# Kernel tuning notes

Measured on AMD Instinct MI355X. Metric: run time of the kernel, lower is better.

Reference implementation:

```python
import jax, jax.numpy as jnp
import numpy as np

B, NLB, NPB, SDIM = 128, 32, 160, 256  # complexes, ligand atoms, pocket CAs, scalar dim


def _uniform(key, shape, fan_in):
    # kaiming_uniform_(a=sqrt(5)) -> U(-1/sqrt(fan_in), 1/sqrt(fan_in))
    bound = 1.0 / np.sqrt(fan_in)
    return jax.random.uniform(key, shape, jnp.float32, -bound, bound)


def setup_inputs() -> dict:
    key = jax.random.key(0)
    k1, k2, k3, k4, k5 = jax.random.split(key, 5)
    NL, NP = B * NLB, B * NPB
    # block-diagonal cross adjacency: every ligand atom paired with every pocket CA
    # of the same complex (same as (batch_ligand[:,None]==batch_pocket[None,:]).nonzero().T)
    l = np.repeat(np.arange(NL, dtype=np.int32), NPB)
    p = (np.arange(B, dtype=np.int32)[:, None, None] * NPB
         + np.zeros((1, NLB, 1), dtype=np.int32)
         + np.arange(NPB, dtype=np.int32)[None, None, :]).reshape(-1)
    return {
        "s_ligand": jax.random.normal(k1, (NL, SDIM), jnp.float32),
        "s_pocket": jax.random.normal(k2, (NP, SDIM), jnp.float32),
        "l": jnp.asarray(l),
        "p": jnp.asarray(p),
        "W1": _uniform(k3, (SDIM // 2, SDIM), SDIM),
        "b1": jnp.zeros((SDIM // 2,), jnp.float32),
        "W2": _uniform(k4, (SDIM // 4, SDIM // 2), SDIM // 2),
        "b2": jnp.zeros((SDIM // 4,), jnp.float32),
        "W3": _uniform(k5, (1, SDIM // 4), SDIM // 4),
        "b3": jnp.zeros((1,), jnp.float32),
    }


def reference(s_ligand, s_pocket, l, p, W1, b1, W2, b2, W3, b3):
    # gather cross-pair embeddings and sum: s[e] = s_ligand[l[e]] + s_pocket[p[e]]
    s = s_ligand[l] + s_pocket[p]                      # [E, sdim]
    h = jax.nn.silu(s @ W1.T + b1)                     # [E, sdim/2]
    h = jax.nn.silu(h @ W2.T + b2)                     # [E, sdim/4]
    out = jax.nn.relu(h @ W3.T + b3)                   # [E, 1]
    return out.squeeze(-1)                             # [E]
```

## Files before the change

kernel.cpp:

```cpp
#include <hip/hip_runtime.h>
#include <hip/hip_bf16.h>


#define B_CPLX   128
#define NLB      32
#define NPB      160
#define SDIM     256
#define H1DIM    128
#define NL_TOT   (B_CPLX * NLB)
#define NP_TOT   (B_CPLX * NPB)
#define NROWS    (NL_TOT + NP_TOT)
#define E_TOT    (B_CPLX * NLB * NPB)

#define W1_LDS_STRIDE 264
#define JT_CHUNK 16
#define ZP_STRIDE 132

typedef __bf16 bf16x8 __attribute__((ext_vector_type(8)));
typedef unsigned short ushortx8 __attribute__((ext_vector_type(8)));
typedef unsigned short ushortx4 __attribute__((ext_vector_type(4)));
typedef unsigned uintx4 __attribute__((ext_vector_type(4)));
typedef float f32x4 __attribute__((ext_vector_type(4)));

__device__ __forceinline__ unsigned short f2bf(float f) {
    unsigned u = __builtin_bit_cast(unsigned, f);
    u += 0x7FFFu + ((u >> 16) & 1u);
    return (unsigned short)(u >> 16);
}

__device__ __forceinline__ unsigned perm_hi16u(unsigned u0, unsigned u1) {
    return __builtin_amdgcn_perm(u1, u0, 0x07060302u);
}

__device__ __forceinline__ unsigned pack2_rhu(float x0, float x1) {
    unsigned u0 = __builtin_bit_cast(unsigned, x0) + 0x8000u;
    unsigned u1 = __builtin_bit_cast(unsigned, x1) + 0x8000u;
    return perm_hi16u(u0, u1);
}

__device__ __forceinline__ bf16x8 pack8_rhu(const float* x) {
    uintx4 h;
#pragma unroll
    for (int j = 0; j < 4; ++j) h[j] = pack2_rhu(x[2 * j], x[2 * j + 1]);
    return __builtin_bit_cast(bf16x8, h);
}

__device__ __forceinline__ void pack_split(const float* x, bf16x8& hi, bf16x8& lo) {
    uintx4 h, l;
#pragma unroll
    for (int j = 0; j < 4; ++j) {
        float x0 = x[2 * j], x1 = x[2 * j + 1];
        unsigned u0 = __builtin_bit_cast(unsigned, x0);
        unsigned u1 = __builtin_bit_cast(unsigned, x1);
        h[j] = perm_hi16u(u0, u1);
        float hf0 = __builtin_bit_cast(float, u0 & 0xFFFF0000u);
        float hf1 = __builtin_bit_cast(float, u1 & 0xFFFF0000u);
        l[j] = pack2_rhu(x0 - hf0, x1 - hf1);
    }
    hi = __builtin_bit_cast(bf16x8, h);
    lo = __builtin_bit_cast(bf16x8, l);
}

__device__ __forceinline__ float fast_silu(float x) {
    return x * __builtin_amdgcn_rcpf(1.0f + __expf(-x));
}

__device__ __forceinline__ float rowsum16(float s) {
    int b;
    b = __builtin_bit_cast(int, s);
    b = __builtin_amdgcn_update_dpp(b, b, 0x121, 0xF, 0xF, false);
    s += __builtin_bit_cast(float, b);
    b = __builtin_bit_cast(int, s);
    b = __builtin_amdgcn_update_dpp(b, b, 0x122, 0xF, 0xF, false);
    s += __builtin_bit_cast(float, b);
    b = __builtin_bit_cast(int, s);
    b = __builtin_amdgcn_update_dpp(b, b, 0x124, 0xF, 0xF, false);
    s += __builtin_bit_cast(float, b);
    b = __builtin_bit_cast(int, s);
    b = __builtin_amdgcn_update_dpp(b, b, 0x128, 0xF, 0xF, false);
    s += __builtin_bit_cast(float, b);
    return s;
}

__global__ __launch_bounds__(256) void proj_kernel(
    const float* __restrict__ s_lig, const float* __restrict__ s_poc,
    const float* __restrict__ W1,    const float* __restrict__ b1,
    float* __restrict__ Z)
{
    __shared__ unsigned short w1s[64 * W1_LDS_STRIDE];

    const int tid  = threadIdx.x;
    const int tg   = blockIdx.x >> 1;
    const int half = blockIdx.x & 1;

    {
        const f32x4* w4 = (const f32x4*)(W1 + (size_t)half * 64 * SDIM);
#pragma unroll
        for (int r = 0; r < 2; ++r) {
            f32x4 t[8];
#pragma unroll
            for (int s = 0; s < 8; ++s) t[s] = w4[tid + (r * 8 + s) * 256];
#pragma unroll
            for (int s = 0; s < 8; ++s) {
                const int u = tid + (r * 8 + s) * 256;
                const int n = u >> 6;
                const int k4 = u & 63;
                ushortx4 us;
#pragma unroll
                for (int j = 0; j < 4; ++j) us[j] = f2bf(t[s][j]);
                *(ushortx4*)(&w1s[n * W1_LDS_STRIDE + k4 * 4]) = us;
            }
        }
    }
    __syncthreads();

    const int lane = tid & 63;
    const int widx = tid >> 6;
    const int c    = lane & 15;
    const int q    = lane >> 4;
    const int tile = tg * 4 + widx;
    const int row  = tile * 16 + c;

    const float* src = (row < NL_TOT) ? (s_lig + (size_t)row * SDIM)
                                      : (s_poc + (size_t)(row - NL_TOT) * SDIM);

    f32x4 acc[4];
#pragma unroll
    for (int nt = 0; nt < 4; ++nt) acc[nt] = (f32x4){0.f, 0.f, 0.f, 0.f};

#pragma unroll
    for (int ks = 0; ks < 8; ++ks) {
        const int k0 = ks * 32 + q * 8;
        f32x4 xa = *reinterpret_cast<const f32x4*>(src + k0);
        f32x4 xb = *reinterpret_cast<const f32x4*>(src + k0 + 4);
        float xv[8] = {xa[0], xa[1], xa[2], xa[3], xb[0], xb[1], xb[2], xb[3]};
        bf16x8 ahi, alo;
        pack_split(xv, ahi, alo);
        bf16x8 bfrag[4];
#pragma unroll
        for (int nt = 0; nt < 4; ++nt)
            bfrag[nt] = *reinterpret_cast<const bf16x8*>(
                &w1s[(nt * 16 + c) * W1_LDS_STRIDE + k0]);
#pragma unroll
        for (int nt = 0; nt < 4; ++nt)
            acc[nt] = __builtin_amdgcn_mfma_f32_16x16x32_bf16(ahi, bfrag[nt], acc[nt], 0, 0, 0);
#pragma unroll
        for (int nt = 0; nt < 4; ++nt)
            acc[nt] = __builtin_amdgcn_mfma_f32_16x16x32_bf16(alo, bfrag[nt], acc[nt], 0, 0, 0);
    }

    const int mb = tile * 16 + q * 4;
#pragma unroll
    for (int nt = 0; nt < 4; ++nt) {
        const int n = half * 64 + nt * 16 + c;
        const float bias = b1[n];
#pragma unroll
        for (int r = 0; r < 4; ++r) {
            const int m = mb + r;
            float v = acc[nt][r];
            if (m < NL_TOT) v += bias;
            Z[(size_t)m * H1DIM + n] = v;
        }
    }
}

__global__ __launch_bounds__(256) void edge_kernel(
    const float* __restrict__ Z,
    const float* __restrict__ W2, const float* __restrict__ b2,
    const float* __restrict__ W3, const float* __restrict__ b3,
    float* __restrict__ out)
{
    __shared__ float zp[JT_CHUNK * ZP_STRIDE];
    __shared__ unsigned short w2s[16 * 64 * 8];

    const int tid = threadIdx.x;
    const int bid = blockIdx.x;
    const int b   = bid / 20;
    const int rem = bid - b * 20;
    const int jt  = rem >> 1;
    const int ih  = rem & 1;

    {
        const float* zpg = Z + (size_t)(NL_TOT + b * NPB + jt * JT_CHUNK) * H1DIM;
#pragma unroll
        for (int s = 0; s < 2; ++s) {
            const int u   = tid + s * 256;
            const int row = u >> 5;
            const int c4  = u & 31;
            f32x4 v = *(const f32x4*)(zpg + (size_t)row * H1DIM + c4 * 4);
            *(f32x4*)(&zp[row * ZP_STRIDE + c4 * 4]) = v;
        }
    }

    {
#pragma unroll
        for (int s = 0; s < 4; ++s) {
            const int slot   = tid + s * 256;
            const int lane_s = slot & 63;
            const int chunk  = slot >> 6;
            const int nt     = chunk >> 2;
            const int ks     = chunk & 3;
            const int n      = nt * 16 + (lane_s & 15);
            const int k0     = ks * 32 + (lane_s >> 4) * 8;
            const float* wsrc = W2 + (size_t)n * H1DIM + k0;
            f32x4 wa = *(const f32x4*)wsrc;
            f32x4 wb = *(const f32x4*)(wsrc + 4);
            float wv[8] = {wa[0], wa[1], wa[2], wa[3], wb[0], wb[1], wb[2], wb[3]};
            ushortx8 us;
#pragma unroll
            for (int j = 0; j < 8; ++j) us[j] = f2bf(wv[j]);
            *(ushortx8*)(&w2s[slot * 8]) = us;
        }
    }

    const int lane = tid & 63;
    const int widx = tid >> 6;
    const int c    = lane & 15;
    const int q    = lane >> 4;

    float b2f[4], w3f[4];
#pragma unroll
    for (int nt = 0; nt < 4; ++nt) {
        b2f[nt] = b2[nt * 16 + c];
        w3f[nt] = W3[nt * 16 + c];
    }
    const float b3v = b3[0];

    __syncthreads();

    const float* lgbase = Z + (size_t)(b * NLB) * H1DIM;
    const float* prow   = &zp[c * ZP_STRIDE];
    const unsigned short* wbase = &w2s[lane * 8];

    const int a0 = ih * 16 + widx * 4;

    f32x4 lgA[4][2], lgB[4][2];
    {
        const float* lr0 = lgbase + (size_t)a0 * H1DIM;
#pragma unroll
        for (int ks = 0; ks < 4; ++ks) {
            const int k0 = ks * 32 + q * 8;
            lgA[ks][0] = *(const f32x4*)(lr0 + k0);
            lgA[ks][1] = *(const f32x4*)(lr0 + k0 + 4);
            lgB[ks][0] = *(const f32x4*)(lr0 + H1DIM + k0);
            lgB[ks][1] = *(const f32x4*)(lr0 + H1DIM + k0 + 4);
        }
    }

#pragma unroll
    for (int pair = 0; pair < 2; ++pair) {
        const int i0 = a0 + pair * 2;

        f32x4 acc0[4], acc1[4];
#pragma unroll
        for (int nt = 0; nt < 4; ++nt) {
            const float bb = b2f[nt];
            acc0[nt] = (f32x4){bb, bb, bb, bb};
            acc1[nt] = (f32x4){bb, bb, bb, bb};
        }

#pragma unroll
        for (int ks = 0; ks < 4; ++ks) {
            const int k0 = ks * 32 + q * 8;
            bf16x8 bfr[4];
#pragma unroll
            for (int nt = 0; nt < 4; ++nt)
                bfr[nt] = *(const bf16x8*)(wbase + (nt * 4 + ks) * 512);
            f32x4 pa = *(const f32x4*)(prow + k0);
            f32x4 pb = *(const f32x4*)(prow + k0 + 4);
            float hv0[8], hv1[8];
#pragma unroll
            for (int j = 0; j < 4; ++j) {
                hv0[j]     = fast_silu(pa[j] + lgA[ks][0][j]);
                hv0[4 + j] = fast_silu(pb[j] + lgA[ks][1][j]);
                hv1[j]     = fast_silu(pa[j] + lgB[ks][0][j]);
                hv1[4 + j] = fast_silu(pb[j] + lgB[ks][1][j]);
            }
            bf16x8 a0f = pack8_rhu(hv0);
            bf16x8 a1f = pack8_rhu(hv1);
#pragma unroll
            for (int nt = 0; nt < 4; ++nt)
                acc0[nt] = __builtin_amdgcn_mfma_f32_16x16x32_bf16(a0f, bfr[nt], acc0[nt], 0, 0, 0);
#pragma unroll
            for (int nt = 0; nt < 4; ++nt)
                acc1[nt] = __builtin_amdgcn_mfma_f32_16x16x32_bf16(a1f, bfr[nt], acc1[nt], 0, 0, 0);
        }

        {
            const float* lrn = lgbase + (size_t)(i0 + 2) * H1DIM;
#pragma unroll
            for (int ks = 0; ks < 4; ++ks) {
                const int k0 = ks * 32 + q * 8;
                lgA[ks][0] = *(const f32x4*)(lrn + k0);
                lgA[ks][1] = *(const f32x4*)(lrn + k0 + 4);
                lgB[ks][0] = *(const f32x4*)(lrn + H1DIM + k0);
                lgB[ks][1] = *(const f32x4*)(lrn + H1DIM + k0 + 4);
            }
        }

#pragma unroll
        for (int at = 0; at < 2; ++at) {
            const f32x4* A = at ? acc1 : acc0;
            float s0 = 0.f, s1 = 0.f, s2 = 0.f, s3 = 0.f;
#pragma unroll
            for (int nt = 0; nt < 4; ++nt) {
                s0 += fast_silu(A[nt][0]) * w3f[nt];
                s1 += fast_silu(A[nt][1]) * w3f[nt];
                s2 += fast_silu(A[nt][2]) * w3f[nt];
                s3 += fast_silu(A[nt][3]) * w3f[nt];
            }
            s0 = rowsum16(s0);
            s1 = rowsum16(s1);
            s2 = rowsum16(s2);
            s3 = rowsum16(s3);
            if (c < 4) {
                float v = (c == 0) ? s0 : (c == 1) ? s1 : (c == 2) ? s2 : s3;
                const int e0 = (b * NLB + i0 + at) * NPB + jt * JT_CHUNK;
                out[e0 + q * 4 + c] = fmaxf(v + b3v, 0.0f);
            }
        }
    }
}

extern "C" void kernel_launch(void* const* d_in, const int* in_sizes, int n_in,
                              void* d_out, int out_size, void* d_ws, size_t ws_size,
                              hipStream_t stream)
{
    const float* s_lig = (const float*)d_in[0];
    const float* s_poc = (const float*)d_in[1];
    const float* W1    = (const float*)d_in[4];
    const float* b1    = (const float*)d_in[5];
    const float* W2    = (const float*)d_in[6];
    const float* b2    = (const float*)d_in[7];
    const float* W3    = (const float*)d_in[8];
    const float* b3    = (const float*)d_in[9];

    float* Z = (float*)d_ws;

    hipLaunchKernelGGL(proj_kernel, dim3(NROWS / 16 / 4 * 2), dim3(256), 0, stream,
                       s_lig, s_poc, W1, b1, Z);
    hipLaunchKernelGGL(edge_kernel, dim3(B_CPLX * 20), dim3(256), 0, stream,
                       Z, W2, b2, W3, b3, (float*)d_out);
}
```

Before: 138.5 us.

## Fuse projection into edge kernel, recomputing per-block W1 projections in registers

Removes the separate projection kernel and the Z workspace round trip. Each edge block now computes its own 16 pocket rows and 16 ligand rows of the first-layer projection with MFMA, reading W1 straight from global memory and converting it to bf16. The results go into shared memory instead of global memory. This saves a launch, the Z write/read traffic and the inter-kernel dependency, but it recomputes the ligand projections about 10x and the pocket projections 2x, and every block re-reads all of W1.

```diff
diff --git a/kernel.cpp b/kernel.cpp
--- a/kernel.cpp
+++ b/kernel.cpp
@@ -9,10 +9,8 @@
 #define H1DIM    128
 #define NL_TOT   (B_CPLX * NLB)
 #define NP_TOT   (B_CPLX * NPB)
-#define NROWS    (NL_TOT + NP_TOT)
 #define E_TOT    (B_CPLX * NLB * NPB)
 
-#define W1_LDS_STRIDE 264
 #define JT_CHUNK 16
 #define ZP_STRIDE 132
 
@@ -82,95 +80,15 @@
     return s;
 }
 
-__global__ __launch_bounds__(256) void proj_kernel(
+__global__ __launch_bounds__(256) void fused_kernel(
     const float* __restrict__ s_lig, const float* __restrict__ s_poc,
     const float* __restrict__ W1,    const float* __restrict__ b1,
-    float* __restrict__ Z)
-{
-    __shared__ unsigned short w1s[64 * W1_LDS_STRIDE];
-
-    const int tid  = threadIdx.x;
-    const int tg   = blockIdx.x >> 1;
-    const int half = blockIdx.x & 1;
-
-    {
-        const f32x4* w4 = (const f32x4*)(W1 + (size_t)half * 64 * SDIM);
-#pragma unroll
-        for (int r = 0; r < 2; ++r) {
-            f32x4 t[8];
-#pragma unroll
-            for (int s = 0; s < 8; ++s) t[s] = w4[tid + (r * 8 + s) * 256];
-#pragma unroll
-            for (int s = 0; s < 8; ++s) {
-                const int u = tid + (r * 8 + s) * 256;
-                const int n = u >> 6;
-                const int k4 = u & 63;
-                ushortx4 us;
-#pragma unroll
-                for (int j = 0; j < 4; ++j) us[j] = f2bf(t[s][j]);
-                *(ushortx4*)(&w1s[n * W1_LDS_STRIDE + k4 * 4]) = us;
-            }
-        }
-    }
-    __syncthreads();
-
-    const int lane = tid & 63;
-    const int widx = tid >> 6;
-    const int c    = lane & 15;
-    const int q    = lane >> 4;
-    const int tile = tg * 4 + widx;
-    const int row  = tile * 16 + c;
-
-    const float* src = (row < NL_TOT) ? (s_lig + (size_t)row * SDIM)
-                                      : (s_poc + (size_t)(row - NL_TOT) * SDIM);
-
-    f32x4 acc[4];
-#pragma unroll
-    for (int nt = 0; nt < 4; ++nt) acc[nt] = (f32x4){0.f, 0.f, 0.f, 0.f};
-
-#pragma unroll
-    for (int ks = 0; ks < 8; ++ks) {
-        const int k0 = ks * 32 + q * 8;
-        f32x4 xa = *reinterpret_cast<const f32x4*>(src + k0);
-        f32x4 xb = *reinterpret_cast<const f32x4*>(src + k0 + 4);
-        float xv[8] = {xa[0], xa[1], xa[2], xa[3], xb[0], xb[1], xb[2], xb[3]};
-        bf16x8 ahi, alo;
-        pack_split(xv, ahi, alo);
-        bf16x8 bfrag[4];
-#pragma unroll
-        for (int nt = 0; nt < 4; ++nt)
-            bfrag[nt] = *reinterpret_cast<const bf16x8*>(
-                &w1s[(nt * 16 + c) * W1_LDS_STRIDE + k0]);
-#pragma unroll
-        for (int nt = 0; nt < 4; ++nt)
-            acc[nt] = __builtin_amdgcn_mfma_f32_16x16x32_bf16(ahi, bfrag[nt], acc[nt], 0, 0, 0);
-#pragma unroll
-        for (int nt = 0; nt < 4; ++nt)
-            acc[nt] = __builtin_amdgcn_mfma_f32_16x16x32_bf16(alo, bfrag[nt], acc[nt], 0, 0, 0);
-    }
-
-    const int mb = tile * 16 + q * 4;
-#pragma unroll
-    for (int nt = 0; nt < 4; ++nt) {
-        const int n = half * 64 + nt * 16 + c;
-        const float bias = b1[n];
-#pragma unroll
-        for (int r = 0; r < 4; ++r) {
-            const int m = mb + r;
-            float v = acc[nt][r];
-            if (m < NL_TOT) v += bias;
-            Z[(size_t)m * H1DIM + n] = v;
-        }
-    }
-}
-
-__global__ __launch_bounds__(256) void edge_kernel(
-    const float* __restrict__ Z,
-    const float* __restrict__ W2, const float* __restrict__ b2,
-    const float* __restrict__ W3, const float* __restrict__ b3,
+    const float* __restrict__ W2,    const float* __restrict__ b2,
+    const float* __restrict__ W3,    const float* __restrict__ b3,
     float* __restrict__ out)
 {
     __shared__ float zp[JT_CHUNK * ZP_STRIDE];
+    __shared__ float zl[JT_CHUNK * ZP_STRIDE];
     __shared__ unsigned short w2s[16 * 64 * 8];
 
     const int tid = threadIdx.x;
@@ -180,17 +98,10 @@
     const int jt  = rem >> 1;
     const int ih  = rem & 1;
 
-    {
-        const float* zpg = Z + (size_t)(NL_TOT + b * NPB + jt * JT_CHUNK) * H1DIM;
-#pragma unroll
-        for (int s = 0; s < 2; ++s) {
-            const int u   = tid + s * 256;
-            const int row = u >> 5;
-            const int c4  = u & 31;
-            f32x4 v = *(const f32x4*)(zpg + (size_t)row * H1DIM + c4 * 4);
-            *(f32x4*)(&zp[row * ZP_STRIDE + c4 * 4]) = v;
-        }
-    }
+    const int lane = tid & 63;
+    const int widx = tid >> 6;
+    const int c    = lane & 15;
+    const int q    = lane >> 4;
 
     {
 #pragma unroll
@@ -213,10 +124,66 @@
         }
     }
 
-    const int lane = tid & 63;
-    const int widx = tid >> 6;
-    const int c    = lane & 15;
-    const int q    = lane >> 4;
+    {
+        const float* xlr = s_lig + (size_t)(b * NLB + ih * 16 + c) * SDIM;
+        const float* xpr = s_poc + (size_t)(b * NPB + jt * JT_CHUNK + c) * SDIM;
+        const float* w1a = W1 + (size_t)(widx * 32 + c) * SDIM;
+        const float* w1b = w1a + (size_t)16 * SDIM;
+
+        f32x4 aP0 = (f32x4){0.f, 0.f, 0.f, 0.f};
+        f32x4 aP1 = (f32x4){0.f, 0.f, 0.f, 0.f};
+        f32x4 aL0 = (f32x4){0.f, 0.f, 0.f, 0.f};
+        f32x4 aL1 = (f32x4){0.f, 0.f, 0.f, 0.f};
+
+#pragma unroll
+        for (int ks = 0; ks < 8; ++ks) {
+            const int k0 = ks * 32 + q * 8;
+            f32x4 wa0 = *(const f32x4*)(w1a + k0);
+            f32x4 wa1 = *(const f32x4*)(w1a + k0 + 4);
+            f32x4 wb0 = *(const f32x4*)(w1b + k0);
+            f32x4 wb1 = *(const f32x4*)(w1b + k0 + 4);
+            ushortx8 u0, u1;
+#pragma unroll
+            for (int j = 0; j < 4; ++j) {
+                u0[j]     = f2bf(wa0[j]);
+                u0[4 + j] = f2bf(wa1[j]);
+                u1[j]     = f2bf(wb0[j]);
+                u1[4 + j] = f2bf(wb1[j]);
+            }
+            const bf16x8 bfr0 = __builtin_bit_cast(bf16x8, u0);
+            const bf16x8 bfr1 = __builtin_bit_cast(bf16x8, u1);
+            f32x4 xa = *(const f32x4*)(xlr + k0);
+            f32x4 xb = *(const f32x4*)(xlr + k0 + 4);
+            float xv[8] = {xa[0], xa[1], xa[2], xa[3], xb[0], xb[1], xb[2], xb[3]};
+            bf16x8 lhi, llo;
+            pack_split(xv, lhi, llo);
+            f32x4 pa = *(const f32x4*)(xpr + k0);
+            f32x4 pb = *(const f32x4*)(xpr + k0 + 4);
+            float pv[8] = {pa[0], pa[1], pa[2], pa[3], pb[0], pb[1], pb[2], pb[3]};
+            bf16x8 phi, plo;
+            pack_split(pv, phi, plo);
+
+            aP0 = __builtin_amdgcn_mfma_f32_16x16x32_bf16(phi, bfr0, aP0, 0, 0, 0);
+            aP1 = __builtin_amdgcn_mfma_f32_16x16x32_bf16(phi, bfr1, aP1, 0, 0, 0);
+            aL0 = __builtin_amdgcn_mfma_f32_16x16x32_bf16(lhi, bfr0, aL0, 0, 0, 0);
+            aL1 = __builtin_amdgcn_mfma_f32_16x16x32_bf16(lhi, bfr1, aL1, 0, 0, 0);
+            aP0 = __builtin_amdgcn_mfma_f32_16x16x32_bf16(plo, bfr0, aP0, 0, 0, 0);
+            aP1 = __builtin_amdgcn_mfma_f32_16x16x32_bf16(plo, bfr1, aP1, 0, 0, 0);
+            aL0 = __builtin_amdgcn_mfma_f32_16x16x32_bf16(llo, bfr0, aL0, 0, 0, 0);
+            aL1 = __builtin_amdgcn_mfma_f32_16x16x32_bf16(llo, bfr1, aL1, 0, 0, 0);
+        }
+
+        const float b10 = b1[widx * 32 + c];
+        const float b11 = b1[widx * 32 + 16 + c];
+#pragma unroll
+        for (int r = 0; r < 4; ++r) {
+            const int row = q * 4 + r;
+            zp[row * ZP_STRIDE + widx * 32 + c]      = aP0[r];
+            zp[row * ZP_STRIDE + widx * 32 + 16 + c] = aP1[r];
+            zl[row * ZP_STRIDE + widx * 32 + c]      = aL0[r] + b10;
+            zl[row * ZP_STRIDE + widx * 32 + 16 + c] = aL1[r] + b11;
+        }
+    }
 
     float b2f[4], w3f[4];
 #pragma unroll
@@ -228,28 +195,25 @@
 
     __syncthreads();
 
-    const float* lgbase = Z + (size_t)(b * NLB) * H1DIM;
-    const float* prow   = &zp[c * ZP_STRIDE];
+    const float* prow = &zp[c * ZP_STRIDE];
     const unsigned short* wbase = &w2s[lane * 8];
 
-    const int a0 = ih * 16 + widx * 4;
-
-    f32x4 lgA[4][2], lgB[4][2];
-    {
-        const float* lr0 = lgbase + (size_t)a0 * H1DIM;
+    const int a0l = widx * 4;
+
+#pragma unroll
+    for (int pair = 0; pair < 2; ++pair) {
+        const int i0 = a0l + pair * 2;
+
+        const float* lr0 = &zl[i0 * ZP_STRIDE];
+        f32x4 lgA[4][2], lgB[4][2];
 #pragma unroll
         for (int ks = 0; ks < 4; ++ks) {
             const int k0 = ks * 32 + q * 8;
             lgA[ks][0] = *(const f32x4*)(lr0 + k0);
             lgA[ks][1] = *(const f32x4*)(lr0 + k0 + 4);
-            lgB[ks][0] = *(const f32x4*)(lr0 + H1DIM + k0);
-            lgB[ks][1] = *(const f32x4*)(lr0 + H1DIM + k0 + 4);
-        }
-    }
-
-#pragma unroll
-    for (int pair = 0; pair < 2; ++pair) {
-        const int i0 = a0 + pair * 2;
+            lgB[ks][0] = *(const f32x4*)(lr0 + ZP_STRIDE + k0);
+            lgB[ks][1] = *(const f32x4*)(lr0 + ZP_STRIDE + k0 + 4);
+        }
 
         f32x4 acc0[4], acc1[4];
 #pragma unroll
@@ -284,18 +248,6 @@
 #pragma unroll
             for (int nt = 0; nt < 4; ++nt)
                 acc1[nt] = __builtin_amdgcn_mfma_f32_16x16x32_bf16(a1f, bfr[nt], acc1[nt], 0, 0, 0);
-        }
-
-        {
-            const float* lrn = lgbase + (size_t)(i0 + 2) * H1DIM;
-#pragma unroll
-            for (int ks = 0; ks < 4; ++ks) {
-                const int k0 = ks * 32 + q * 8;
-                lgA[ks][0] = *(const f32x4*)(lrn + k0);
-                lgA[ks][1] = *(const f32x4*)(lrn + k0 + 4);
-                lgB[ks][0] = *(const f32x4*)(lrn + H1DIM + k0);
-                lgB[ks][1] = *(const f32x4*)(lrn + H1DIM + k0 + 4);
-            }
         }
 
 #pragma unroll
@@ -315,7 +267,7 @@
             s3 = rowsum16(s3);
             if (c < 4) {
                 float v = (c == 0) ? s0 : (c == 1) ? s1 : (c == 2) ? s2 : s3;
-                const int e0 = (b * NLB + i0 + at) * NPB + jt * JT_CHUNK;
+                const int e0 = (b * NLB + ih * 16 + i0 + at) * NPB + jt * JT_CHUNK;
                 out[e0 + q * 4 + c] = fmaxf(v + b3v, 0.0f);
             }
         }
@@ -335,10 +287,8 @@
     const float* W3    = (const float*)d_in[8];
     const float* b3    = (const float*)d_in[9];
 
-    float* Z = (float*)d_ws;
-
-    hipLaunchKernelGGL(proj_kernel, dim3(NROWS / 16 / 4 * 2), dim3(256), 0, stream,
-                       s_lig, s_poc, W1, b1, Z);
-    hipLaunchKernelGGL(edge_kernel, dim3(B_CPLX * 20), dim3(256), 0, stream,
-                       Z, W2, b2, W3, b3, (float*)d_out);
-}
+    (void)d_ws; (void)ws_size;
+
+    hipLaunchKernelGGL(fused_kernel, dim3(B_CPLX * 20), dim3(256), 0, stream,
+                       s_lig, s_poc, W1, b1, W2, b2, W3, b3, (float*)d_out);
+}
```

Result: slower. 169.9 us (+22.7%).

## Make edge kernel persistent over work items with prefetched pocket tiles

Applied to the files above, without the earlier changes.

The edge kernel previously launched one block per (complex, pocket tile, ligand half), so every block converted W2 to bf16 in LDS and processed only two ligand-row pairs. It now launches a fifth as many blocks, each looping over five consecutive work items of eight ligand rows by one pocket tile. The W2 conversion is amortized across items, and the next item's pocket tile and ligand rows are prefetched into registers during the current MFMA work. The cost is two extra block barriers whenever the pocket tile changes, plus fewer blocks for latency hiding.

```diff
diff --git a/kernel.cpp b/kernel.cpp
--- a/kernel.cpp
+++ b/kernel.cpp
@@ -15,6 +15,10 @@
 #define W1_LDS_STRIDE 264
 #define JT_CHUNK 16
 #define ZP_STRIDE 132
+
+#define NITEMS        (B_CPLX * 10 * 4)
+#define NITEM_PER_BLK 5
+#define EDGE_BLOCKS   (NITEMS / NITEM_PER_BLK)
 
 typedef __bf16 bf16x8 __attribute__((ext_vector_type(8)));
 typedef unsigned short ushortx8 __attribute__((ext_vector_type(8)));
@@ -174,23 +178,6 @@
     __shared__ unsigned short w2s[16 * 64 * 8];
 
     const int tid = threadIdx.x;
-    const int bid = blockIdx.x;
-    const int b   = bid / 20;
-    const int rem = bid - b * 20;
-    const int jt  = rem >> 1;
-    const int ih  = rem & 1;
-
-    {
-        const float* zpg = Z + (size_t)(NL_TOT + b * NPB + jt * JT_CHUNK) * H1DIM;
-#pragma unroll
-        for (int s = 0; s < 2; ++s) {
-            const int u   = tid + s * 256;
-            const int row = u >> 5;
-            const int c4  = u & 31;
-            f32x4 v = *(const f32x4*)(zpg + (size_t)row * H1DIM + c4 * 4);
-            *(f32x4*)(&zp[row * ZP_STRIDE + c4 * 4]) = v;
-        }
-    }
 
     {
 #pragma unroll
@@ -226,17 +213,26 @@
     }
     const float b3v = b3[0];
 
-    __syncthreads();
-
-    const float* lgbase = Z + (size_t)(b * NLB) * H1DIM;
-    const float* prow   = &zp[c * ZP_STRIDE];
-    const unsigned short* wbase = &w2s[lane * 8];
-
-    const int a0 = ih * 16 + widx * 4;
+    int id = blockIdx.x * NITEM_PER_BLK;
+    int b  = id / 40;
+    int rr = id - b * 40;
+    int jt = rr >> 2;
+    int g  = rr & 3;
+
+    const int u0 = tid, u1 = tid + 256;
+
+    f32x4 zr0, zr1;
+    {
+        const float* zpg = Z + (size_t)(NL_TOT + b * NPB + jt * JT_CHUNK) * H1DIM;
+        zr0 = *(const f32x4*)(zpg + (size_t)(u0 >> 5) * H1DIM + (u0 & 31) * 4);
+        zr1 = *(const f32x4*)(zpg + (size_t)(u1 >> 5) * H1DIM + (u1 & 31) * 4);
+        *(f32x4*)(&zp[(u0 >> 5) * ZP_STRIDE + (u0 & 31) * 4]) = zr0;
+        *(f32x4*)(&zp[(u1 >> 5) * ZP_STRIDE + (u1 & 31) * 4]) = zr1;
+    }
 
     f32x4 lgA[4][2], lgB[4][2];
     {
-        const float* lr0 = lgbase + (size_t)a0 * H1DIM;
+        const float* lr0 = Z + (size_t)(b * NLB + g * 8 + widx * 2) * H1DIM;
 #pragma unroll
         for (int ks = 0; ks < 4; ++ks) {
             const int k0 = ks * 32 + q * 8;
@@ -247,9 +243,27 @@
         }
     }
 
-#pragma unroll
-    for (int pair = 0; pair < 2; ++pair) {
-        const int i0 = a0 + pair * 2;
+    __syncthreads();
+
+    const float* prow = &zp[c * ZP_STRIDE];
+    const unsigned short* wbase = &w2s[lane * 8];
+
+    for (int it = 0; it < NITEM_PER_BLK; ++it) {
+        int bn = b, jtn = jt, gn = g;
+        bool sc = false;
+        if (it < NITEM_PER_BLK - 1) {
+            const int idn = id + 1;
+            bn = idn / 40;
+            const int rn = idn - bn * 40;
+            jtn = rn >> 2;
+            gn  = rn & 3;
+            sc  = (jtn != jt) || (bn != b);
+            if (sc) {
+                const float* zpg = Z + (size_t)(NL_TOT + bn * NPB + jtn * JT_CHUNK) * H1DIM;
+                zr0 = *(const f32x4*)(zpg + (size_t)(u0 >> 5) * H1DIM + (u0 & 31) * 4);
+                zr1 = *(const f32x4*)(zpg + (size_t)(u1 >> 5) * H1DIM + (u1 & 31) * 4);
+            }
+        }
 
         f32x4 acc0[4], acc1[4];
 #pragma unroll
@@ -286,8 +300,8 @@
                 acc1[nt] = __builtin_amdgcn_mfma_f32_16x16x32_bf16(a1f, bfr[nt], acc1[nt], 0, 0, 0);
         }
 
-        {
-            const float* lrn = lgbase + (size_t)(i0 + 2) * H1DIM;
+        if (it < NITEM_PER_BLK - 1) {
+            const float* lrn = Z + (size_t)(bn * NLB + gn * 8 + widx * 2) * H1DIM;
 #pragma unroll
             for (int ks = 0; ks < 4; ++ks) {
                 const int k0 = ks * 32 + q * 8;
@@ -315,10 +329,19 @@
             s3 = rowsum16(s3);
             if (c < 4) {
                 float v = (c == 0) ? s0 : (c == 1) ? s1 : (c == 2) ? s2 : s3;
-                const int e0 = (b * NLB + i0 + at) * NPB + jt * JT_CHUNK;
+                const int e0 = (b * NLB + g * 8 + widx * 2 + at) * NPB + jt * JT_CHUNK;
                 out[e0 + q * 4 + c] = fmaxf(v + b3v, 0.0f);
             }
         }
+
+        if (sc) {
+            __syncthreads();
+            *(f32x4*)(&zp[(u0 >> 5) * ZP_STRIDE + (u0 & 31) * 4]) = zr0;
+            *(f32x4*)(&zp[(u1 >> 5) * ZP_STRIDE + (u1 & 31) * 4]) = zr1;
+            __syncthreads();
+        }
+
+        id += 1; b = bn; jt = jtn; g = gn;
     }
 }
 
@@ -339,6 +362,6 @@
 
     hipLaunchKernelGGL(proj_kernel, dim3(NROWS / 16 / 4 * 2), dim3(256), 0, stream,
                        s_lig, s_poc, W1, b1, Z);
-    hipLaunchKernelGGL(edge_kernel, dim3(B_CPLX * 20), dim3(256), 0, stream,
+    hipLaunchKernelGGL(edge_kernel, dim3(EDGE_BLOCKS), dim3(256), 0, stream,
                        Z, W2, b2, W3, b3, (float*)d_out);
 }
```

Measured after the change: 141.6 us. 2.2% more time.

## Keep W2 fragments in registers and stream edge work items per wave

Applied to the files above, without the earlier changes.

The edge kernel drops the LDS staging of pocket rows and W2. Each wave now loads its W2 bf16 fragments straight into registers and works through a flat list of 10 (complex, pocket tile, ligand atom) items. The next ligand row is prefetched, and pocket rows are reloaded only when the tile changes. This removes LDS traffic and block-wide syncs and makes the grid smaller, but it adds register pressure from 16 held fragments and loses the two-row interleave of MFMA chains.

```diff
diff --git a/kernel.cpp b/kernel.cpp
--- a/kernel.cpp
+++ b/kernel.cpp
@@ -14,7 +14,10 @@
 
 #define W1_LDS_STRIDE 264
 #define JT_CHUNK 16
-#define ZP_STRIDE 132
+
+#define ITEMS_PER_WAVE 10
+#define NITEMS        (B_CPLX * 10 * NLB)
+#define EDGE_BLOCKS   (NITEMS / ITEMS_PER_WAVE / 4)
 
 typedef __bf16 bf16x8 __attribute__((ext_vector_type(8)));
 typedef unsigned short ushortx8 __attribute__((ext_vector_type(8)));
@@ -170,54 +173,29 @@
     const float* __restrict__ W3, const float* __restrict__ b3,
     float* __restrict__ out)
 {
-    __shared__ float zp[JT_CHUNK * ZP_STRIDE];
-    __shared__ unsigned short w2s[16 * 64 * 8];
-
-    const int tid = threadIdx.x;
-    const int bid = blockIdx.x;
-    const int b   = bid / 20;
-    const int rem = bid - b * 20;
-    const int jt  = rem >> 1;
-    const int ih  = rem & 1;
-
-    {
-        const float* zpg = Z + (size_t)(NL_TOT + b * NPB + jt * JT_CHUNK) * H1DIM;
-#pragma unroll
-        for (int s = 0; s < 2; ++s) {
-            const int u   = tid + s * 256;
-            const int row = u >> 5;
-            const int c4  = u & 31;
-            f32x4 v = *(const f32x4*)(zpg + (size_t)row * H1DIM + c4 * 4);
-            *(f32x4*)(&zp[row * ZP_STRIDE + c4 * 4]) = v;
-        }
-    }
-
-    {
-#pragma unroll
-        for (int s = 0; s < 4; ++s) {
-            const int slot   = tid + s * 256;
-            const int lane_s = slot & 63;
-            const int chunk  = slot >> 6;
-            const int nt     = chunk >> 2;
-            const int ks     = chunk & 3;
-            const int n      = nt * 16 + (lane_s & 15);
-            const int k0     = ks * 32 + (lane_s >> 4) * 8;
-            const float* wsrc = W2 + (size_t)n * H1DIM + k0;
-            f32x4 wa = *(const f32x4*)wsrc;
-            f32x4 wb = *(const f32x4*)(wsrc + 4);
-            float wv[8] = {wa[0], wa[1], wa[2], wa[3], wb[0], wb[1], wb[2], wb[3]};
-            ushortx8 us;
-#pragma unroll
-            for (int j = 0; j < 8; ++j) us[j] = f2bf(wv[j]);
-            *(ushortx8*)(&w2s[slot * 8]) = us;
-        }
-    }
-
+    const int tid  = threadIdx.x;
     const int lane = tid & 63;
     const int widx = tid >> 6;
     const int c    = lane & 15;
     const int q    = lane >> 4;
 
+    bf16x8 wfr[16];
+#pragma unroll
+    for (int f = 0; f < 16; ++f) {
+        const int nt = f >> 2;
+        const int ks = f & 3;
+        const float* wsrc = W2 + (size_t)(nt * 16 + c) * H1DIM + ks * 32 + q * 8;
+        f32x4 wa = *(const f32x4*)wsrc;
+        f32x4 wb = *(const f32x4*)(wsrc + 4);
+        ushortx8 us;
+#pragma unroll
+        for (int j = 0; j < 4; ++j) {
+            us[j]     = f2bf(wa[j]);
+            us[4 + j] = f2bf(wb[j]);
+        }
+        wfr[f] = __builtin_bit_cast(bf16x8, us);
+    }
+
     float b2f[4], w3f[4];
 #pragma unroll
     for (int nt = 0; nt < 4; ++nt) {
@@ -226,88 +204,89 @@
     }
     const float b3v = b3[0];
 
-    __syncthreads();
-
-    const float* lgbase = Z + (size_t)(b * NLB) * H1DIM;
-    const float* prow   = &zp[c * ZP_STRIDE];
-    const unsigned short* wbase = &w2s[lane * 8];
-
-    const int a0 = ih * 16 + widx * 4;
-
-    f32x4 lgA[4][2], lgB[4][2];
+    int id = (blockIdx.x * 4 + widx) * ITEMS_PER_WAVE;
+    int b  = id / 320;
+    int rr = id - b * 320;
+    int jt = rr >> 5;
+    int at = rr & 31;
+
+    f32x4 pk[4][2];
     {
-        const float* lr0 = lgbase + (size_t)a0 * H1DIM;
+        const float* pkg = Z + (size_t)(NL_TOT + b * NPB + jt * JT_CHUNK + c) * H1DIM;
 #pragma unroll
         for (int ks = 0; ks < 4; ++ks) {
             const int k0 = ks * 32 + q * 8;
-            lgA[ks][0] = *(const f32x4*)(lr0 + k0);
-            lgA[ks][1] = *(const f32x4*)(lr0 + k0 + 4);
-            lgB[ks][0] = *(const f32x4*)(lr0 + H1DIM + k0);
-            lgB[ks][1] = *(const f32x4*)(lr0 + H1DIM + k0 + 4);
-        }
-    }
-
-#pragma unroll
-    for (int pair = 0; pair < 2; ++pair) {
-        const int i0 = a0 + pair * 2;
-
-        f32x4 acc0[4], acc1[4];
+            pk[ks][0] = *(const f32x4*)(pkg + k0);
+            pk[ks][1] = *(const f32x4*)(pkg + k0 + 4);
+        }
+    }
+
+    f32x4 lr[4][2];
+    {
+        const float* lrg = Z + (size_t)(b * NLB + at) * H1DIM;
+#pragma unroll
+        for (int ks = 0; ks < 4; ++ks) {
+            const int k0 = ks * 32 + q * 8;
+            lr[ks][0] = *(const f32x4*)(lrg + k0);
+            lr[ks][1] = *(const f32x4*)(lrg + k0 + 4);
+        }
+    }
+
+    for (int it = 0; it < ITEMS_PER_WAVE; ++it) {
+        f32x4 acc[4];
 #pragma unroll
         for (int nt = 0; nt < 4; ++nt) {
             const float bb = b2f[nt];
-            acc0[nt] = (f32x4){bb, bb, bb, bb};
-            acc1[nt] = (f32x4){bb, bb, bb, bb};
+            acc[nt] = (f32x4){bb, bb, bb, bb};
         }
 
 #pragma unroll
         for (int ks = 0; ks < 4; ++ks) {
-            const int k0 = ks * 32 + q * 8;
-            bf16x8 bfr[4];
+            float hv[8];
+#pragma unroll
+            for (int j = 0; j < 4; ++j) {
+                hv[j]     = fast_silu(pk[ks][0][j] + lr[ks][0][j]);
+                hv[4 + j] = fast_silu(pk[ks][1][j] + lr[ks][1][j]);
+            }
+            bf16x8 af = pack8_rhu(hv);
 #pragma unroll
             for (int nt = 0; nt < 4; ++nt)
-                bfr[nt] = *(const bf16x8*)(wbase + (nt * 4 + ks) * 512);
-            f32x4 pa = *(const f32x4*)(prow + k0);
-            f32x4 pb = *(const f32x4*)(prow + k0 + 4);
-            float hv0[8], hv1[8];
-#pragma unroll
-            for (int j = 0; j < 4; ++j) {
-                hv0[j]     = fast_silu(pa[j] + lgA[ks][0][j]);
-                hv0[4 + j] = fast_silu(pb[j] + lgA[ks][1][j]);
-                hv1[j]     = fast_silu(pa[j] + lgB[ks][0][j]);
-                hv1[4 + j] = fast_silu(pb[j] + lgB[ks][1][j]);
-            }
-            bf16x8 a0f = pack8_rhu(hv0);
-            bf16x8 a1f = pack8_rhu(hv1);
-#pragma unroll
-            for (int nt = 0; nt < 4; ++nt)
-                acc0[nt] = __builtin_amdgcn_mfma_f32_16x16x32_bf16(a0f, bfr[nt], acc0[nt], 0, 0, 0);
-#pragma unroll
-            for (int nt = 0; nt < 4; ++nt)
-                acc1[nt] = __builtin_amdgcn_mfma_f32_16x16x32_bf16(a1f, bfr[nt], acc1[nt], 0, 0, 0);
-        }
-
-        {
-            const float* lrn = lgbase + (size_t)(i0 + 2) * H1DIM;
+                acc[nt] = __builtin_amdgcn_mfma_f32_16x16x32_bf16(af, wfr[nt * 4 + ks], acc[nt], 0, 0, 0);
+        }
+
+        int bn = b, jtn = jt, atn = at;
+        if (it != ITEMS_PER_WAVE - 1) {
+            const int idn = id + 1;
+            bn = idn / 320;
+            const int rn = idn - bn * 320;
+            jtn = rn >> 5;
+            atn = rn & 31;
+            const float* lrn = Z + (size_t)(bn * NLB + atn) * H1DIM;
 #pragma unroll
             for (int ks = 0; ks < 4; ++ks) {
                 const int k0 = ks * 32 + q * 8;
-                lgA[ks][0] = *(const f32x4*)(lrn + k0);
-                lgA[ks][1] = *(const f32x4*)(lrn + k0 + 4);
-                lgB[ks][0] = *(const f32x4*)(lrn + H1DIM + k0);
-                lgB[ks][1] = *(const f32x4*)(lrn + H1DIM + k0 + 4);
-            }
-        }
-
-#pragma unroll
-        for (int at = 0; at < 2; ++at) {
-            const f32x4* A = at ? acc1 : acc0;
+                lr[ks][0] = *(const f32x4*)(lrn + k0);
+                lr[ks][1] = *(const f32x4*)(lrn + k0 + 4);
+            }
+            if (jtn != jt || bn != b) {
+                const float* pkn = Z + (size_t)(NL_TOT + bn * NPB + jtn * JT_CHUNK + c) * H1DIM;
+#pragma unroll
+                for (int ks = 0; ks < 4; ++ks) {
+                    const int k0 = ks * 32 + q * 8;
+                    pk[ks][0] = *(const f32x4*)(pkn + k0);
+                    pk[ks][1] = *(const f32x4*)(pkn + k0 + 4);
+                }
+            }
+        }
+
+        {
             float s0 = 0.f, s1 = 0.f, s2 = 0.f, s3 = 0.f;
 #pragma unroll
             for (int nt = 0; nt < 4; ++nt) {
-                s0 += fast_silu(A[nt][0]) * w3f[nt];
-                s1 += fast_silu(A[nt][1]) * w3f[nt];
-                s2 += fast_silu(A[nt][2]) * w3f[nt];
-                s3 += fast_silu(A[nt][3]) * w3f[nt];
+                s0 += fast_silu(acc[nt][0]) * w3f[nt];
+                s1 += fast_silu(acc[nt][1]) * w3f[nt];
+                s2 += fast_silu(acc[nt][2]) * w3f[nt];
+                s3 += fast_silu(acc[nt][3]) * w3f[nt];
             }
             s0 = rowsum16(s0);
             s1 = rowsum16(s1);
@@ -315,10 +294,12 @@
             s3 = rowsum16(s3);
             if (c < 4) {
                 float v = (c == 0) ? s0 : (c == 1) ? s1 : (c == 2) ? s2 : s3;
-                const int e0 = (b * NLB + i0 + at) * NPB + jt * JT_CHUNK;
+                const int e0 = (b * NLB + at) * NPB + jt * JT_CHUNK;
                 out[e0 + q * 4 + c] = fmaxf(v + b3v, 0.0f);
             }
         }
+
+        id += 1; b = bn; jt = jtn; at = atn;
     }
 }
 
@@ -339,6 +320,6 @@
 
     hipLaunchKernelGGL(proj_kernel, dim3(NROWS / 16 / 4 * 2), dim3(256), 0, stream,
                        s_lig, s_poc, W1, b1, Z);
-    hipLaunchKernelGGL(edge_kernel, dim3(B_CPLX * 20), dim3(256), 0, stream,
+    hipLaunchKernelGGL(edge_kernel, dim3(EDGE_BLOCKS), dim3(256), 0, stream,
                        Z, W2, b2, W3, b3, (float*)d_out);
 }
```

Result: slower. 149.0 us (+7.6%).
